# Performance work log

Measured on AMD Instinct MI355X. Metric: run time of the kernel, lower is better.

The kernel has to match this reference:

```python
import jax, jax.numpy as jnp
import numpy as np

B, C, H, W = 32, 512, 56, 56
P = 64  # planes = C / ratio
EPS = 1e-3


def setup_inputs() -> dict:
    key = jax.random.key(0)
    ks = jax.random.split(key, 10)
    return {
        "x": jax.random.normal(ks[0], (B, C, H, W), jnp.float32),
        "wm": jax.random.normal(ks[1], (1, C), jnp.float32) * 0.05,
        "bm": jax.random.normal(ks[2], (1,), jnp.float32) * 0.05,
        "w1": jax.random.normal(ks[3], (P, C), jnp.float32) * 0.05,
        "b1": jax.random.normal(ks[4], (P,), jnp.float32) * 0.05,
        "ln_g": jax.random.normal(ks[5], (P,), jnp.float32) * 0.1 + 1.0,
        "ln_b": jax.random.normal(ks[6], (P,), jnp.float32) * 0.05,
        "w2": jax.random.normal(ks[7], (C, P), jnp.float32) * 0.05,
        "b2": jax.random.normal(ks[8], (C,), jnp.float32) * 0.05,
        "gamma": jax.random.normal(ks[9], (1,), jnp.float32) * 0.1,
    }


def reference(x, wm, bm, w1, b1, ln_g, ln_b, w2, b2, gamma):
    b, c, h, w = x.shape
    xf = x.reshape(b, c, h * w)                       # (B, C, S)
    # attention spatial pool: 1x1 conv mask -> softmax over spatial -> weighted sum
    mask = jnp.einsum('bcs,c->bs', xf, wm[0]) + bm[0]  # (B, S)
    attn = jax.nn.softmax(mask, axis=-1)               # softmax over H*W
    context = jnp.einsum('bcs,bs->bc', xf, attn)       # (B, C)
    # channel_add_conv: 1x1 conv -> LayerNorm([P,1,1], eps=1e-3) -> ReLU -> 1x1 conv
    hid = jnp.einsum('pc,bc->bp', w1, context) + b1    # (B, P)
    mu = hid.mean(axis=-1, keepdims=True)
    var = jnp.mean((hid - mu) ** 2, axis=-1, keepdims=True)
    hid = (hid - mu) / jnp.sqrt(var + EPS) * ln_g + ln_b
    hid = jax.nn.relu(hid)
    add = jnp.einsum('cp,bp->bc', w2, hid) + b2        # (B, C)
    return x + gamma[0] * add[:, :, None, None]
```

## Files before the change

kernel.cpp:

```cpp
#include <hip/hip_runtime.h>

constexpr int kB = 32;
constexpr int kC = 512;
constexpr int kS = 56 * 56;
constexpr int kP = 64;
constexpr float kEps = 1e-3f;

constexpr int kST = 64;
constexpr int kNB = kS / kST;
static_assert(kS % kST == 0, "tile must divide S");

typedef float f4v __attribute__((ext_vector_type(4)));

__global__ __launch_bounds__(512, 4)
void k_fused_pass(const float* __restrict__ x, const float* __restrict__ wm,
                  float* __restrict__ pc, float* __restrict__ pmz) {
    __shared__ float swm[kC];
    __shared__ f4v   pmw4[8][16];
    __shared__ f4v   es4[kST / 4];

    const int b    = blockIdx.y;
    const int tile = blockIdx.x;
    const int s0   = tile * kST;
    const int t    = threadIdx.x;
    const int si   = t & 15;
    const int c0   = t >> 4;
    const int w    = t >> 6;
    const int l    = t & 63;

    swm[t & (kC - 1)] = wm[t & (kC - 1)];
    __syncthreads();

    const float* xb = x + (size_t)b * kC * kS + s0 + si * 4;

    f4v xt[16];
#pragma unroll
    for (int j = 0; j < 16; ++j)
        xt[j] = *(const f4v*)(xb + (size_t)(c0 + 32 * j) * kS);

    float m0 = 0.f, m1 = 0.f, m2 = 0.f, m3 = 0.f;
#pragma unroll
    for (int j = 0; j < 16; ++j) {
        const float wv = swm[c0 + 32 * j];
        m0 += xt[j].x * wv; m1 += xt[j].y * wv;
        m2 += xt[j].z * wv; m3 += xt[j].w * wv;
    }
#pragma unroll
    for (int off = 16; off <= 32; off <<= 1) {
        m0 += __shfl_xor(m0, off); m1 += __shfl_xor(m1, off);
        m2 += __shfl_xor(m2, off); m3 += __shfl_xor(m3, off);
    }
    if (l < 16) pmw4[w][si] = (f4v){m0, m1, m2, m3};
    __syncthreads();

    if (t < kST) {
        const float* pmf = (const float*)pmw4;
        float v = 0.f;
#pragma unroll
        for (int ww = 0; ww < 8; ++ww) v += pmf[ww * kST + t];
        float mx = v;
#pragma unroll
        for (int off = 1; off < 64; off <<= 1) mx = fmaxf(mx, __shfl_xor(mx, off));
        const float e = expf(v - mx);
        float z = e;
#pragma unroll
        for (int off = 1; off < 64; off <<= 1) z += __shfl_xor(z, off);
        ((float*)es4)[t] = e;
        if (t == 0) {
            pmz[(b * kNB + tile) * 2 + 0] = mx;
            pmz[(b * kNB + tile) * 2 + 1] = z;
        }
    }
    __syncthreads();

    const f4v e4 = es4[si];
    float* pco = pc + ((size_t)b * kNB + tile) * kC;
#pragma unroll
    for (int j = 0; j < 16; ++j) {
        float a = xt[j].x * e4.x + xt[j].y * e4.y + xt[j].z * e4.z + xt[j].w * e4.w;
        a += __shfl_xor(a, 1); a += __shfl_xor(a, 2);
        a += __shfl_xor(a, 4); a += __shfl_xor(a, 8);
        if (si == 0) pco[c0 + 32 * j] = a;
    }
}

__global__ __launch_bounds__(512)
void k_combine_mlp(const float* __restrict__ pc, const float* __restrict__ pmz,
                   const float* __restrict__ w1, const float* __restrict__ b1,
                   const float* __restrict__ ln_g, const float* __restrict__ ln_b,
                   const float* __restrict__ w2, const float* __restrict__ b2,
                   float* __restrict__ add) {
    const int b = blockIdx.x;
    const int t = threadIdx.x;
    __shared__ float scale[kNB];
    __shared__ float ctx[kC];
    __shared__ float hp[kP][9];
    __shared__ float hid[kP];

    if (t < 64) {
        const float m1 = (t < kNB) ? pmz[(b * kNB + t) * 2] : -INFINITY;
        float m = m1;
        for (int off = 32; off; off >>= 1) m = fmaxf(m, __shfl_xor(m, off));
        const float e1 = (t < kNB) ? expf(m1 - m) : 0.f;
        float z = 0.f;
        if (t < kNB) z = pmz[(b * kNB + t) * 2 + 1] * e1;
        for (int off = 32; off; off >>= 1) z += __shfl_xor(z, off);
        const float inv = 1.f / z;
        if (t < kNB) scale[t] = e1 * inv;
    }
    __syncthreads();

    {
        float acc = 0.f;
        for (int i = 0; i < kNB; ++i)
            acc += pc[((size_t)b * kNB + i) * kC + t] * scale[i];
        ctx[t] = acc;
    }
    __syncthreads();

    {
        const int p = t & 63, k = t >> 6;
        const float* w1p = w1 + p * kC + k * 64;
        const float* cxp = ctx + k * 64;
        float acc = 0.f;
#pragma unroll 8
        for (int i = 0; i < 64; ++i) acc += w1p[i] * cxp[i];
        hp[p][k] = acc;
    }
    __syncthreads();

    if (t < 64) {
        float h = b1[t];
#pragma unroll
        for (int k = 0; k < 8; ++k) h += hp[t][k];
        float mu = h;
        for (int off = 32; off; off >>= 1) mu += __shfl_xor(mu, off);
        mu *= (1.f / kP);
        const float d = h - mu;
        float var = d * d;
        for (int off = 32; off; off >>= 1) var += __shfl_xor(var, off);
        var *= (1.f / kP);
        const float hv = d * rsqrtf(var + kEps) * ln_g[t] + ln_b[t];
        hid[t] = fmaxf(hv, 0.f);
    }
    __syncthreads();

    {
        float a = b2[t];
        const float* w2c = w2 + t * kP;
#pragma unroll
        for (int p = 0; p < kP; ++p) a += w2c[p] * hid[p];
        add[b * kC + t] = a;
    }
}

__global__ __launch_bounds__(256)
void k_out(const float* __restrict__ x, const float* __restrict__ add,
           const float* __restrict__ gamma, float* __restrict__ out) {
    const size_t i4 = (size_t)blockIdx.x * blockDim.x + threadIdx.x;
    const size_t n4 = (size_t)kB * kC * kS / 4;
    if (i4 >= n4) return;
    const int bc = (int)(i4 / (kS / 4));
    const float a = gamma[0] * add[bc];
    f4v xv = ((const f4v*)x)[i4];
    f4v o = {xv.x + a, xv.y + a, xv.z + a, xv.w + a};
    __builtin_nontemporal_store(o, (f4v*)out + i4);
}

extern "C" void kernel_launch(void* const* d_in, const int* in_sizes, int n_in,
                              void* d_out, int out_size, void* d_ws, size_t ws_size,
                              hipStream_t stream) {
    const float* x     = (const float*)d_in[0];
    const float* wm    = (const float*)d_in[1];
    const float* w1    = (const float*)d_in[3];
    const float* b1    = (const float*)d_in[4];
    const float* ln_g  = (const float*)d_in[5];
    const float* ln_b  = (const float*)d_in[6];
    const float* w2    = (const float*)d_in[7];
    const float* b2    = (const float*)d_in[8];
    const float* gamma = (const float*)d_in[9];
    float* out = (float*)d_out;

    float* ws  = (float*)d_ws;
    float* pc  = ws;
    float* pmz = pc + (size_t)kB * kNB * kC;
    float* add = pmz + (size_t)kB * kNB * 2;

    k_fused_pass<<<dim3(kNB, kB), 512, 0, stream>>>(x, wm, pc, pmz);
    k_combine_mlp<<<kB, 512, 0, stream>>>(pc, pmz, w1, b1, ln_g, ln_b, w2, b2, add);

    const size_t n4 = (size_t)kB * kC * kS / 4;
    k_out<<<(unsigned)((n4 + 255) / 256), 256, 0, stream>>>(x, add, gamma, out);
}
```

Baseline: 397.6 us.

## Restructure pool pass into per-wave spatial groups and unroll output kernel

The first pass now runs one wave per 32-position spatial group, two waves per block. Each wave handles the whole channel reduction and its softmax partials on its own, with no shared-memory cross-wave reduction and no block barriers. Instead of holding all of x in registers, it reads x twice (once for the mask, once for the weighted context), relying on cache for the second read. The combine kernel handles twice as many partial groups and folds gamma into add. The output kernel processes 16 float4 per thread and uses normal stores instead of nontemporal ones. Together these trade register pressure and synchronisation for extra global or cache reads and a larger partial buffer.

```diff
diff --git a/kernel.cpp b/kernel.cpp
--- a/kernel.cpp
+++ b/kernel.cpp
@@ -6,81 +6,66 @@
 constexpr int kP = 64;
 constexpr float kEps = 1e-3f;
 
-constexpr int kST = 64;
-constexpr int kNB = kS / kST;
-static_assert(kS % kST == 0, "tile must divide S");
+constexpr int kSG = 32;
+constexpr int kNG = kS / kSG;
+constexpr int kGPB = 2;
+static_assert(kS % kSG == 0, "group must divide S");
+static_assert(kNG % kGPB == 0, "block must divide groups");
 
 typedef float f4v __attribute__((ext_vector_type(4)));
 
-__global__ __launch_bounds__(512, 4)
-void k_fused_pass(const float* __restrict__ x, const float* __restrict__ wm,
-                  float* __restrict__ pc, float* __restrict__ pmz) {
+__global__ __launch_bounds__(128)
+void k_pass_a(const float* __restrict__ x, const float* __restrict__ wm,
+              float* __restrict__ pc, float* __restrict__ pmz) {
     __shared__ float swm[kC];
-    __shared__ f4v   pmw4[8][16];
-    __shared__ f4v   es4[kST / 4];
-
-    const int b    = blockIdx.y;
-    const int tile = blockIdx.x;
-    const int s0   = tile * kST;
-    const int t    = threadIdx.x;
-    const int si   = t & 15;
-    const int c0   = t >> 4;
-    const int w    = t >> 6;
-    const int l    = t & 63;
-
-    swm[t & (kC - 1)] = wm[t & (kC - 1)];
+    const int t = threadIdx.x;
+    swm[t]       = wm[t];
+    swm[t + 128] = wm[t + 128];
+    swm[t + 256] = wm[t + 256];
+    swm[t + 384] = wm[t + 384];
     __syncthreads();
 
-    const float* xb = x + (size_t)b * kC * kS + s0 + si * 4;
+    const int b  = blockIdx.y;
+    const int g  = blockIdx.x * kGPB + (t >> 6);
+    const int l  = t & 63;
+    const int si = l & 7;
+    const int cg = l >> 3;
+    const int s0 = g * kSG;
 
-    f4v xt[16];
-#pragma unroll
-    for (int j = 0; j < 16; ++j)
-        xt[j] = *(const f4v*)(xb + (size_t)(c0 + 32 * j) * kS);
+    const float* xb = x + (size_t)b * kC * kS + (size_t)cg * kS + s0 + si * 4;
 
     float m0 = 0.f, m1 = 0.f, m2 = 0.f, m3 = 0.f;
-#pragma unroll
-    for (int j = 0; j < 16; ++j) {
-        const float wv = swm[c0 + 32 * j];
-        m0 += xt[j].x * wv; m1 += xt[j].y * wv;
-        m2 += xt[j].z * wv; m3 += xt[j].w * wv;
+#pragma unroll 8
+    for (int k = 0; k < 64; ++k) {
+        const f4v v = *(const f4v*)(xb + (size_t)8 * k * kS);
+        const float wv = swm[cg + 8 * k];
+        m0 += v.x * wv; m1 += v.y * wv; m2 += v.z * wv; m3 += v.w * wv;
     }
 #pragma unroll
-    for (int off = 16; off <= 32; off <<= 1) {
+    for (int off = 8; off <= 32; off <<= 1) {
         m0 += __shfl_xor(m0, off); m1 += __shfl_xor(m1, off);
         m2 += __shfl_xor(m2, off); m3 += __shfl_xor(m3, off);
     }
-    if (l < 16) pmw4[w][si] = (f4v){m0, m1, m2, m3};
-    __syncthreads();
+    float mm = fmaxf(fmaxf(m0, m1), fmaxf(m2, m3));
+    mm = fmaxf(mm, __shfl_xor(mm, 1));
+    mm = fmaxf(mm, __shfl_xor(mm, 2));
+    mm = fmaxf(mm, __shfl_xor(mm, 4));
+    const float e0 = expf(m0 - mm), e1 = expf(m1 - mm);
+    const float e2 = expf(m2 - mm), e3 = expf(m3 - mm);
+    float z = e0 + e1 + e2 + e3;
+    z += __shfl_xor(z, 1); z += __shfl_xor(z, 2); z += __shfl_xor(z, 4);
+    if (l == 0) {
+        pmz[(b * kNG + g) * 2 + 0] = mm;
+        pmz[(b * kNG + g) * 2 + 1] = z;
+    }
 
-    if (t < kST) {
-        const float* pmf = (const float*)pmw4;
-        float v = 0.f;
-#pragma unroll
-        for (int ww = 0; ww < 8; ++ww) v += pmf[ww * kST + t];
-        float mx = v;
-#pragma unroll
-        for (int off = 1; off < 64; off <<= 1) mx = fmaxf(mx, __shfl_xor(mx, off));
-        const float e = expf(v - mx);
-        float z = e;
-#pragma unroll
-        for (int off = 1; off < 64; off <<= 1) z += __shfl_xor(z, off);
-        ((float*)es4)[t] = e;
-        if (t == 0) {
-            pmz[(b * kNB + tile) * 2 + 0] = mx;
-            pmz[(b * kNB + tile) * 2 + 1] = z;
-        }
-    }
-    __syncthreads();
-
-    const f4v e4 = es4[si];
-    float* pco = pc + ((size_t)b * kNB + tile) * kC;
-#pragma unroll
-    for (int j = 0; j < 16; ++j) {
-        float a = xt[j].x * e4.x + xt[j].y * e4.y + xt[j].z * e4.z + xt[j].w * e4.w;
-        a += __shfl_xor(a, 1); a += __shfl_xor(a, 2);
-        a += __shfl_xor(a, 4); a += __shfl_xor(a, 8);
-        if (si == 0) pco[c0 + 32 * j] = a;
+    float* pco = pc + ((size_t)b * kNG + g) * kC;
+#pragma unroll 8
+    for (int k = 0; k < 64; ++k) {
+        const f4v v = *(const f4v*)(xb + (size_t)8 * k * kS);
+        float p = v.x * e0 + v.y * e1 + v.z * e2 + v.w * e3;
+        p += __shfl_xor(p, 1); p += __shfl_xor(p, 2); p += __shfl_xor(p, 4);
+        if (si == 0) pco[cg + 8 * k] = p;
     }
 }
 
@@ -89,31 +74,35 @@
                    const float* __restrict__ w1, const float* __restrict__ b1,
                    const float* __restrict__ ln_g, const float* __restrict__ ln_b,
                    const float* __restrict__ w2, const float* __restrict__ b2,
-                   float* __restrict__ add) {
+                   const float* __restrict__ gamma, float* __restrict__ add) {
     const int b = blockIdx.x;
     const int t = threadIdx.x;
-    __shared__ float scale[kNB];
+    __shared__ float scale[kNG];
     __shared__ float ctx[kC];
     __shared__ float hp[kP][9];
     __shared__ float hid[kP];
 
     if (t < 64) {
-        const float m1 = (t < kNB) ? pmz[(b * kNB + t) * 2] : -INFINITY;
-        float m = m1;
+        const float m1 = (t      < kNG) ? pmz[(b * kNG + t     ) * 2] : -INFINITY;
+        const float m2 = (t + 64 < kNG) ? pmz[(b * kNG + t + 64) * 2] : -INFINITY;
+        float m = fmaxf(m1, m2);
         for (int off = 32; off; off >>= 1) m = fmaxf(m, __shfl_xor(m, off));
-        const float e1 = (t < kNB) ? expf(m1 - m) : 0.f;
+        const float e1 = (t      < kNG) ? expf(m1 - m) : 0.f;
+        const float e2 = (t + 64 < kNG) ? expf(m2 - m) : 0.f;
         float z = 0.f;
-        if (t < kNB) z = pmz[(b * kNB + t) * 2 + 1] * e1;
+        if (t      < kNG) z += pmz[(b * kNG + t     ) * 2 + 1] * e1;
+        if (t + 64 < kNG) z += pmz[(b * kNG + t + 64) * 2 + 1] * e2;
         for (int off = 32; off; off >>= 1) z += __shfl_xor(z, off);
         const float inv = 1.f / z;
-        if (t < kNB) scale[t] = e1 * inv;
+        if (t      < kNG) scale[t]      = e1 * inv;
+        if (t + 64 < kNG) scale[t + 64] = e2 * inv;
     }
     __syncthreads();
 
     {
         float acc = 0.f;
-        for (int i = 0; i < kNB; ++i)
-            acc += pc[((size_t)b * kNB + i) * kC + t] * scale[i];
+        for (int i = 0; i < kNG; ++i)
+            acc += pc[((size_t)b * kNG + i) * kC + t] * scale[i];
         ctx[t] = acc;
     }
     __syncthreads();
@@ -150,21 +139,25 @@
         const float* w2c = w2 + t * kP;
 #pragma unroll
         for (int p = 0; p < kP; ++p) a += w2c[p] * hid[p];
-        add[b * kC + t] = a;
+        add[b * kC + t] = gamma[0] * a;
     }
 }
 
+constexpr int kOutBlocks = (kB * kC * kS / 4) / (256 * 16);
+static_assert(kOutBlocks * 256 * 16 == kB * kC * kS / 4, "exact tiling");
+
 __global__ __launch_bounds__(256)
-void k_out(const float* __restrict__ x, const float* __restrict__ add,
-           const float* __restrict__ gamma, float* __restrict__ out) {
-    const size_t i4 = (size_t)blockIdx.x * blockDim.x + threadIdx.x;
-    const size_t n4 = (size_t)kB * kC * kS / 4;
-    if (i4 >= n4) return;
-    const int bc = (int)(i4 / (kS / 4));
-    const float a = gamma[0] * add[bc];
-    f4v xv = ((const f4v*)x)[i4];
-    f4v o = {xv.x + a, xv.y + a, xv.z + a, xv.w + a};
-    __builtin_nontemporal_store(o, (f4v*)out + i4);
+void k_out(const float* __restrict__ x, const float* __restrict__ addv,
+           float* __restrict__ out) {
+    const size_t base = (size_t)blockIdx.x * 4096 + threadIdx.x;
+#pragma unroll
+    for (int j = 0; j < 16; ++j) {
+        const size_t i4 = base + (size_t)j * 256;
+        const float a = addv[i4 / (kS / 4)];
+        const f4v xv = ((const f4v*)x)[i4];
+        const f4v o = {xv.x + a, xv.y + a, xv.z + a, xv.w + a};
+        ((f4v*)out)[i4] = o;
+    }
 }
 
 extern "C" void kernel_launch(void* const* d_in, const int* in_sizes, int n_in,
@@ -183,12 +176,11 @@
 
     float* ws  = (float*)d_ws;
     float* pc  = ws;
-    float* pmz = pc + (size_t)kB * kNB * kC;
-    float* add = pmz + (size_t)kB * kNB * 2;
+    float* pmz = pc + (size_t)kB * kNG * kC;
+    float* add = pmz + (size_t)kB * kNG * 2;
 
-    k_fused_pass<<<dim3(kNB, kB), 512, 0, stream>>>(x, wm, pc, pmz);
-    k_combine_mlp<<<kB, 512, 0, stream>>>(pc, pmz, w1, b1, ln_g, ln_b, w2, b2, add);
-
-    const size_t n4 = (size_t)kB * kC * kS / 4;
-    k_out<<<(unsigned)((n4 + 255) / 256), 256, 0, stream>>>(x, add, gamma, out);
+    k_pass_a<<<dim3(kNG / kGPB, kB), kGPB * 64, 0, stream>>>(x, wm, pc, pmz);
+    k_combine_mlp<<<kB, 512, 0, stream>>>(pc, pmz, w1, b1, ln_g, ln_b,
+                                          w2, b2, gamma, add);
+    k_out<<<kOutBlocks, 256, 0, stream>>>(x, add, out);
 }
```

After: 437.2 us. 1.1x slower.
